# Optimization experiments

Hardware: AMD Instinct MI355X
Metric: run time of the kernel (lower is better)

Reference implementation:

```python
import jax, jax.numpy as jnp
import numpy as np

EPS = 0.25  # diffusion-map epsilon

def setup_inputs() -> dict:
    key = jax.random.key(0)
    ks = jax.random.split(key, 6)
    B, N, F, L = 8, 2048, 256, 16
    s = lambda fan_in: 1.0 / np.sqrt(fan_in)
    return {
        "x":      jax.random.normal(ks[0], (B, N, F), dtype=jnp.float32),
        "proj_w": jax.random.normal(ks[1], (L, F), dtype=jnp.float32) * s(F),
        "proj_b": jnp.zeros((L,), dtype=jnp.float32),
        "pi_w1":  jax.random.normal(ks[2], (F, L), dtype=jnp.float32) * s(L),
        "pi_b1":  jnp.zeros((F,), dtype=jnp.float32),
        "pi_w2":  jax.random.normal(ks[3], (1, F), dtype=jnp.float32) * s(F),
        "pi_b2":  jnp.zeros((1,), dtype=jnp.float32),
        "dt":     jnp.array([0.1], dtype=jnp.float32),
    }

def reference(x, proj_w, proj_b, pi_w1, pi_b1, pi_w2, pi_b2, dt):
    # z = proj(x): [B, N, L]
    z = jnp.einsum("bnf,lf->bnl", x, proj_w) + proj_b
    # pairwise squared distances via expansion (avoids [B,N,N,L] intermediate)
    sq = jnp.sum(z * z, axis=-1)                              # [B, N]
    gram = jnp.einsum("bnl,bml->bnm", z, z)                   # [B, N, N]
    d2 = jnp.maximum(sq[:, :, None] + sq[:, None, :] - 2.0 * gram, 0.0)
    K = jnp.exp(-d2 / (4.0 * EPS))                            # K_epsilon [B,N,N]
    q = jnp.sum(K, axis=2)                                    # q_epsilon_tilde [B,N]
    # pi(z): MLP 16 -> 256 -> 1 with ReLU then Sigmoid
    h = jax.nn.relu(jnp.einsum("bnl,fl->bnf", z, pi_w1) + pi_b1)
    pi_v = jax.nn.sigmoid(jnp.einsum("bnf,of->bno", h, pi_w2) + pi_b2)[..., 0]  # [B,N]
    # K_tilde = K @ diag(pi/q): scale columns
    Kt = K * (pi_v / q)[:, None, :]                            # [B,N,N]
    row = jnp.sum(Kt, axis=2) + 1e-5                           # diag of D_tilde
    # L = (1/eps) * D_tilde^{-1} K_tilde - I ; inverse of diagonal = reciprocal
    # L @ x computed without materializing identity:
    Lx = (1.0 / EPS) * jnp.einsum("bnm,bmf->bnf", Kt / row[:, :, None], x) - x
    return x + dt[0] * Lx
```

## Files before the change

### kernel.cpp

```cpp
#include <hip/hip_runtime.h>
#include <hip/hip_bf16.h>

#define BATCH 8
#define NN    2048
#define FF    256
#define LL    16

typedef float f32x4 __attribute__((ext_vector_type(4)));
typedef short s16x8 __attribute__((ext_vector_type(8)));

static __device__ __forceinline__ unsigned short f2bf(float f) {
    return __builtin_bit_cast(unsigned short, __float2bfloat16(f));
}
static __device__ __forceinline__ float bf2f(unsigned short u) {
    unsigned int x = ((unsigned int)u) << 16;
    return __builtin_bit_cast(float, x);
}

__global__ __launch_bounds__(256) void fused_a_kernel(
    const float* __restrict__ x,
    const float* __restrict__ proj_w, const float* __restrict__ proj_b,
    const float* __restrict__ pi_w1,  const float* __restrict__ pi_b1,
    const float* __restrict__ pi_w2,  const float* __restrict__ pi_b2,
    unsigned short* __restrict__ xT,
    unsigned short* __restrict__ zbG,
    float* __restrict__ sqbuf,
    float* __restrict__ pibuf)
{
    const int bid = blockIdx.x;
    const int b = bid & 7, nt = bid >> 3;
    const int n0 = nt * 32;
    const int t = threadIdx.x;
    const int wv = t >> 6, ln = t & 63;
    const int kg = ln >> 4, cl = ln & 15;

    const float* xb = x + (size_t)b * NN * FF;
    unsigned short* xTb = xT + (size_t)b * FF * NN;

    __shared__ unsigned short xbsh[32 * 264];
    __shared__ unsigned short Wbsh[16 * 264];
    __shared__ unsigned short W1bsh[256 * 24];
    __shared__ unsigned short zbsh[32 * 24];
    __shared__ float b1sh[256], w2sh[256], pbsh[16];
    __shared__ float pp[2][32];

#pragma unroll
    for (int i = 0; i < 8; ++i) {
        const int slot = i * 256 + t;
        const int r = slot >> 6, c4 = slot & 63;
        const float4 v = *(const float4*)(xb + (size_t)(n0 + r) * FF + c4 * 4);
        ushort4 o; o.x = f2bf(v.x); o.y = f2bf(v.y); o.z = f2bf(v.z); o.w = f2bf(v.w);
        *(ushort4*)&xbsh[r * 264 + c4 * 4] = o;
    }
#pragma unroll
    for (int i = 0; i < 4; ++i) {
        const int slot = i * 256 + t;
        const int l = slot >> 6, c4 = slot & 63;
        const float4 v = *(const float4*)(proj_w + l * FF + c4 * 4);
        ushort4 o; o.x = f2bf(v.x); o.y = f2bf(v.y); o.z = f2bf(v.z); o.w = f2bf(v.w);
        *(ushort4*)&Wbsh[l * 264 + c4 * 4] = o;
    }
#pragma unroll
    for (int i = 0; i < 4; ++i) {
        const int slot = i * 256 + t;
        const int f = slot >> 2, q = slot & 3;
        const float4 v = *(const float4*)(pi_w1 + f * LL + q * 4);
        ushort4 o; o.x = f2bf(v.x); o.y = f2bf(v.y); o.z = f2bf(v.z); o.w = f2bf(v.w);
        *(ushort4*)&W1bsh[f * 24 + q * 4] = o;
    }
    b1sh[t] = pi_b1[t];
    w2sh[t] = pi_w2[t];
    if (t < 16) pbsh[t] = proj_b[t];
    __syncthreads();

    if (wv < 2) {
        f32x4 zacc = {0.f, 0.f, 0.f, 0.f};
#pragma unroll
        for (int g = 0; g < 8; ++g) {
            const s16x8 af = *(const s16x8*)&xbsh[(wv * 16 + cl) * 264 + g * 32 + kg * 8];
            const s16x8 bf = *(const s16x8*)&Wbsh[cl * 264 + g * 32 + kg * 8];
            zacc = __builtin_amdgcn_mfma_f32_16x16x32_bf16(af, bf, zacc, 0, 0, 0);
        }
        const float pb = pbsh[cl];
#pragma unroll
        for (int r = 0; r < 4; ++r)
            zbsh[(wv * 16 + kg * 4 + r) * 24 + cl] = f2bf(zacc[r] + pb);
    }
    __syncthreads();

    if (t < 32) {
        unsigned short zr[16]; float sq = 0.f;
#pragma unroll
        for (int l = 0; l < 16; ++l) {
            zr[l] = zbsh[t * 24 + l];
            const float zf = bf2f(zr[l]);
            sq = fmaf(zf, zf, sq);
        }
        unsigned short* dst = zbG + ((size_t)b * NN + n0 + t) * 16;
        *(uint4*)dst = *(uint4*)&zr[0];
        *(uint4*)(dst + 8) = *(uint4*)&zr[8];
        sqbuf[(size_t)b * NN + n0 + t] = sq;
    }

    {
        const int ntl = wv & 1;
        s16x8 bz = {0, 0, 0, 0, 0, 0, 0, 0};
        if (kg < 2) bz = *(const s16x8*)&zbsh[(ntl * 16 + cl) * 24 + kg * 8];
        float pisum = 0.f;
        const f32x4 zf4 = {0.f, 0.f, 0.f, 0.f};
#pragma unroll
        for (int j = 0; j < 8; ++j) {
            const int ft = (wv >> 1) * 8 + j;
            s16x8 aw = {0, 0, 0, 0, 0, 0, 0, 0};
            if (kg < 2) aw = *(const s16x8*)&W1bsh[(ft * 16 + cl) * 24 + kg * 8];
            const f32x4 h4 = __builtin_amdgcn_mfma_f32_16x16x32_bf16(aw, bz, zf4, 0, 0, 0);
#pragma unroll
            for (int r = 0; r < 4; ++r) {
                const int f = ft * 16 + kg * 4 + r;
                const float h = fmaxf(h4[r] + b1sh[f], 0.f);
                pisum = fmaf(h, w2sh[f], pisum);
            }
        }
        pisum += __shfl_xor(pisum, 16, 64);
        pisum += __shfl_xor(pisum, 32, 64);
        if (ln < 16) pp[wv >> 1][ntl * 16 + ln] = pisum;
    }
    __syncthreads();

    if (t < 32) {
        const float tp = pp[0][t] + pp[1][t] + pi_b2[0];
        pibuf[(size_t)b * NN + n0 + t] = 1.f / (1.f + __expf(-tp));
    }

#pragma unroll
    for (int it = 0; it < 8; ++it) {
        const int f = wv * 64 + it * 8 + (ln >> 3);
        const int q = ln & 7;
        ushort4 o;
        o.x = xbsh[(q * 4 + 0) * 264 + f];
        o.y = xbsh[(q * 4 + 1) * 264 + f];
        o.z = xbsh[(q * 4 + 2) * 264 + f];
        o.w = xbsh[(q * 4 + 3) * 264 + f];
        *(ushort4*)(xTb + (size_t)f * NN + n0 + q * 4) = o;
    }
}

__global__ __launch_bounds__(256) void qc_kernel(
    const unsigned short* __restrict__ zbG,
    const float* __restrict__ sqbuf,
    const float* __restrict__ pibuf,
    float* __restrict__ cbuf)
{
    const int bid = blockIdx.x;
    const int b = bid & 7, nt = bid >> 3;
    const int n0 = nt * 32;
    const int t = threadIdx.x;
    const int wv = t >> 6, ln = t & 63;
    const int kg = ln >> 4, cl = ln & 15;

    const unsigned short* zb = zbG + (size_t)b * NN * LL;
    const float* sqb = sqbuf + (size_t)b * NN;
    __shared__ float qq[2][32];

    s16x8 zn = {0, 0, 0, 0, 0, 0, 0, 0};
    if (kg < 2) zn = *(const s16x8*)(zb + (size_t)(n0 + (wv & 1) * 16 + cl) * 16 + kg * 8);
    const float sqn = sqb[n0 + (wv & 1) * 16 + cl];
    const f32x4 zf4 = {0.f, 0.f, 0.f, 0.f};
    float qloc = 0.f;

#pragma unroll 2
    for (int ch = 0; ch < 32; ++ch) {
#pragma unroll
        for (int mi = 0; mi < 2; ++mi) {
            const int mm = ch * 64 + ((wv >> 1) + mi * 2) * 16;
            s16x8 zm = {0, 0, 0, 0, 0, 0, 0, 0};
            if (kg < 2) zm = *(const s16x8*)(zb + (size_t)(mm + cl) * 16 + kg * 8);
            const f32x4 sqm4 = *(const f32x4*)(sqb + mm + kg * 4);
            const f32x4 g = __builtin_amdgcn_mfma_f32_16x16x32_bf16(zm, zn, zf4, 0, 0, 0);
#pragma unroll
            for (int r = 0; r < 4; ++r)
                qloc += __expf(2.f * g[r] - sqm4[r] - sqn);
        }
    }
    qloc += __shfl_xor(qloc, 16, 64);
    qloc += __shfl_xor(qloc, 32, 64);
    if (ln < 16) qq[wv >> 1][(wv & 1) * 16 + ln] = qloc;
    __syncthreads();
    if (t < 32) {
        const size_t gi = (size_t)b * NN + n0 + t;
        cbuf[gi] = pibuf[gi] / (qq[0][t] + qq[1][t]);
    }
}

struct MRegs {
    s16x8 zm0, zm1;
    f32x4 sqm0, sqm1, cm0, cm1;
    s16x8 a0, a1, a2, a3;
};

__global__ __launch_bounds__(512) void main_kernel(
    const float* __restrict__ x,
    const unsigned short* __restrict__ xT,
    const unsigned short* __restrict__ zbG,
    const float* __restrict__ sqbuf,
    const float* __restrict__ cbuf,
    const float* __restrict__ dtp,
    float* __restrict__ out)
{
    const int bid = blockIdx.x;
    const int b = bid & 7, nt = bid >> 3;
    const int n0 = nt * 64;
    const int t = threadIdx.x;
    const int wv = t >> 6, ln = t & 63;
    const int kg = ln >> 4, cl = ln & 15;
    const int nt4 = wv >> 1;
    const int mgrp = wv & 1;

    const float*          xb  = x   + (size_t)b * NN * FF;
    const unsigned short* xTb = xT  + (size_t)b * FF * NN;
    const unsigned short* zb  = zbG + (size_t)b * NN * LL;
    const float*          sqB = sqbuf + (size_t)b * NN;
    const float*          cB  = cbuf  + (size_t)b * NN;
    float*                ob  = out + (size_t)b * NN * FF;

    __shared__ unsigned short wsh[2][64][64];
    __shared__ float rsp[2][64];

    const float dtv = dtp[0];
    const int nloc = nt4 * 16 + cl;

    s16x8 zn = {0, 0, 0, 0, 0, 0, 0, 0};
    if (kg < 2) zn = *(const s16x8*)(zb + (size_t)(n0 + nloc) * 16 + kg * 8);
    const float sqn = sqB[n0 + nloc];
    const f32x4 zf4 = {0.f, 0.f, 0.f, 0.f};

    f32x4 acc[2][4];
#pragma unroll
    for (int fi = 0; fi < 2; ++fi)
#pragma unroll
        for (int ni = 0; ni < 4; ++ni) acc[fi][ni] = (f32x4){0.f, 0.f, 0.f, 0.f};
    float rloc = 0.f;

    auto PRE = [&](MRegs& R, int kt) {
        const int m0 = kt * 64;
        const int mmA = m0 + (mgrp * 2 + 0) * 16;
        const int mmB = m0 + (mgrp * 2 + 1) * 16;
        R.zm0 = (s16x8){0, 0, 0, 0, 0, 0, 0, 0};
        R.zm1 = (s16x8){0, 0, 0, 0, 0, 0, 0, 0};
        if (kg < 2) {
            R.zm0 = *(const s16x8*)(zb + (size_t)(mmA + cl) * 16 + kg * 8);
            R.zm1 = *(const s16x8*)(zb + (size_t)(mmB + cl) * 16 + kg * 8);
        }
        R.sqm0 = *(const f32x4*)(sqB + mmA + kg * 4);
        R.sqm1 = *(const f32x4*)(sqB + mmB + kg * 4);
        R.cm0  = *(const f32x4*)(cB + mmA + kg * 4);
        R.cm1  = *(const f32x4*)(cB + mmB + kg * 4);
        const unsigned short* xr0 = xTb + (size_t)(wv * 32 + cl) * NN + m0;
        const unsigned short* xr1 = xTb + (size_t)(wv * 32 + 16 + cl) * NN + m0;
        R.a0 = *(const s16x8*)(xr0 + kg * 8);
        R.a1 = *(const s16x8*)(xr1 + kg * 8);
        R.a2 = *(const s16x8*)(xr0 + 32 + kg * 8);
        R.a3 = *(const s16x8*)(xr1 + 32 + kg * 8);
    };

    auto P1 = [&](const MRegs& R, int cur) {
        char* wb = (char*)wsh + cur * 8192;
#pragma unroll
        for (int j = 0; j < 2; ++j) {
            const s16x8 zm  = j ? R.zm1  : R.zm0;
            const f32x4 sqm = j ? R.sqm1 : R.sqm0;
            const f32x4 cm  = j ? R.cm1  : R.cm0;
            const int mt = mgrp * 2 + j;
            const f32x4 g = __builtin_amdgcn_mfma_f32_16x16x32_bf16(zm, zn, zf4, 0, 0, 0);
            const float w0 = __expf(2.f * g[0] - sqm[0] - sqn) * cm[0];
            const float w1 = __expf(2.f * g[1] - sqm[1] - sqn) * cm[1];
            const float w2 = __expf(2.f * g[2] - sqm[2] - sqn) * cm[2];
            const float w3 = __expf(2.f * g[3] - sqm[3] - sqn) * cm[3];
            rloc += (w0 + w1) + (w2 + w3);
            uint2 val;
            val.x = (unsigned)f2bf(w0) | ((unsigned)f2bf(w1) << 16);
            val.y = (unsigned)f2bf(w2) | ((unsigned)f2bf(w3) << 16);
            const int c16 = mt * 2 + (kg >> 1);
            const int phys = c16 ^ (nloc & 7);
            *(uint2*)(wb + nloc * 128 + phys * 16 + (kg & 1) * 8) = val;
        }
    };

    auto P2 = [&](const MRegs& R, int cur) {
        const char* wb = (const char*)wsh + cur * 8192;
#pragma unroll
        for (int ks = 0; ks < 2; ++ks) {
            s16x8 bw[4];
#pragma unroll
            for (int ni = 0; ni < 4; ++ni) {
                const int nr = ni * 16 + cl;
                const int phys = (ks * 4 + kg) ^ (nr & 7);
                bw[ni] = *(const s16x8*)(wb + nr * 128 + phys * 16);
            }
            const s16x8 aA = ks ? R.a2 : R.a0;
            const s16x8 aB = ks ? R.a3 : R.a1;
#pragma unroll
            for (int ni = 0; ni < 4; ++ni) {
                acc[0][ni] = __builtin_amdgcn_mfma_f32_16x16x32_bf16(aA, bw[ni], acc[0][ni], 0, 0, 0);
                acc[1][ni] = __builtin_amdgcn_mfma_f32_16x16x32_bf16(aB, bw[ni], acc[1][ni], 0, 0, 0);
            }
        }
    };

    MRegs rA, rB;
    PRE(rA, 0);
    for (int kt2 = 0; kt2 < 32; kt2 += 2) {
        PRE(rB, kt2 + 1);
        P1(rA, 0);
        __syncthreads();
        P2(rA, 0);
        if (kt2 + 2 < 32) PRE(rA, kt2 + 2);
        P1(rB, 1);
        __syncthreads();
        P2(rB, 1);
    }

    rloc += __shfl_xor(rloc, 16, 64);
    rloc += __shfl_xor(rloc, 32, 64);
    if (ln < 16) rsp[mgrp][nt4 * 16 + ln] = rloc;
    __syncthreads();

#pragma unroll
    for (int ni = 0; ni < 4; ++ni) {
        const int nl = ni * 16 + cl;
        const float rstot = rsp[0][nl] + rsp[1][nl] + 1e-5f;
        const float sc = 4.f * dtv / rstot;
        const int ng = n0 + nl;
#pragma unroll
        for (int fi = 0; fi < 2; ++fi) {
            const int fg = wv * 32 + fi * 16 + kg * 4;
            const float4 xv = *(const float4*)(xb + (size_t)ng * FF + fg);
            float4 o;
            o.x = (1.f - dtv) * xv.x + sc * acc[fi][ni][0];
            o.y = (1.f - dtv) * xv.y + sc * acc[fi][ni][1];
            o.z = (1.f - dtv) * xv.z + sc * acc[fi][ni][2];
            o.w = (1.f - dtv) * xv.w + sc * acc[fi][ni][3];
            *(float4*)(ob + (size_t)ng * FF + fg) = o;
        }
    }
}

extern "C" void kernel_launch(void* const* d_in, const int* in_sizes, int n_in,
                              void* d_out, int out_size, void* d_ws, size_t ws_size,
                              hipStream_t stream) {
    const float* x      = (const float*)d_in[0];
    const float* proj_w = (const float*)d_in[1];
    const float* proj_b = (const float*)d_in[2];
    const float* pi_w1  = (const float*)d_in[3];
    const float* pi_b1  = (const float*)d_in[4];
    const float* pi_w2  = (const float*)d_in[5];
    const float* pi_b2  = (const float*)d_in[6];
    const float* dtp    = (const float*)d_in[7];
    float* out = (float*)d_out;

    unsigned short* xT  = (unsigned short*)d_ws;
    unsigned short* zbG = xT + (size_t)BATCH * FF * NN;
    float* sqbuf = (float*)(zbG + (size_t)BATCH * NN * LL);
    float* pibuf = sqbuf + (size_t)BATCH * NN;
    float* cbuf  = pibuf + (size_t)BATCH * NN;

    fused_a_kernel<<<dim3(BATCH * (NN / 32)), dim3(256), 0, stream>>>(
        x, proj_w, proj_b, pi_w1, pi_b1, pi_w2, pi_b2, xT, zbG, sqbuf, pibuf);

    qc_kernel<<<dim3(BATCH * (NN / 32)), dim3(256), 0, stream>>>(
        zbG, sqbuf, pibuf, cbuf);

    main_kernel<<<dim3(BATCH * (NN / 64)), dim3(512), 0, stream>>>(
        x, xT, zbG, sqbuf, cbuf, dtp, out);
}
```

Measured before the change: 153.8 us.

## Split main kernel over feature halves, stage xT via async global-to-LDS loads

The main kernel now runs twice as many 256-thread blocks, each covering 128 of the 256 features. Each block stages xT tiles into swizzled LDS with global_load_lds and raises wave priority around the MFMA phase. The qc kernel double-buffers z and squared norms through LDS instead of reading them per tile from global memory. The fused_a kernel pads its LDS rows and moves the transpose write onto the otherwise idle waves. The cost is that every block recomputes the full kernel weights and row sums for its rows, doubling the exp work in the main kernel.

```diff
diff --git a/kernel.cpp b/kernel.cpp
--- a/kernel.cpp
+++ b/kernel.cpp
@@ -15,6 +15,12 @@
 static __device__ __forceinline__ float bf2f(unsigned short u) {
     unsigned int x = ((unsigned int)u) << 16;
     return __builtin_bit_cast(float, x);
+}
+
+typedef const __attribute__((address_space(1))) unsigned int glb_uint;
+typedef __attribute__((address_space(3))) unsigned int lds_uint;
+static __device__ __forceinline__ void gload_lds16(const void* g, void* l) {
+    __builtin_amdgcn_global_load_lds((glb_uint*)g, (lds_uint*)l, 16, 0, 0);
 }
 
 __global__ __launch_bounds__(256) void fused_a_kernel(
@@ -37,8 +43,8 @@
     const float* xb = x + (size_t)b * NN * FF;
     unsigned short* xTb = xT + (size_t)b * FF * NN;
 
-    __shared__ unsigned short xbsh[32 * 264];
-    __shared__ unsigned short Wbsh[16 * 264];
+    __shared__ unsigned short xbsh[32 * 268];
+    __shared__ unsigned short Wbsh[16 * 268];
     __shared__ unsigned short W1bsh[256 * 24];
     __shared__ unsigned short zbsh[32 * 24];
     __shared__ float b1sh[256], w2sh[256], pbsh[16];
@@ -50,7 +56,7 @@
         const int r = slot >> 6, c4 = slot & 63;
         const float4 v = *(const float4*)(xb + (size_t)(n0 + r) * FF + c4 * 4);
         ushort4 o; o.x = f2bf(v.x); o.y = f2bf(v.y); o.z = f2bf(v.z); o.w = f2bf(v.w);
-        *(ushort4*)&xbsh[r * 264 + c4 * 4] = o;
+        *(ushort4*)&xbsh[r * 268 + c4 * 4] = o;
     }
 #pragma unroll
     for (int i = 0; i < 4; ++i) {
@@ -58,7 +64,7 @@
         const int l = slot >> 6, c4 = slot & 63;
         const float4 v = *(const float4*)(proj_w + l * FF + c4 * 4);
         ushort4 o; o.x = f2bf(v.x); o.y = f2bf(v.y); o.z = f2bf(v.z); o.w = f2bf(v.w);
-        *(ushort4*)&Wbsh[l * 264 + c4 * 4] = o;
+        *(ushort4*)&Wbsh[l * 268 + c4 * 4] = o;
     }
 #pragma unroll
     for (int i = 0; i < 4; ++i) {
@@ -77,14 +83,26 @@
         f32x4 zacc = {0.f, 0.f, 0.f, 0.f};
 #pragma unroll
         for (int g = 0; g < 8; ++g) {
-            const s16x8 af = *(const s16x8*)&xbsh[(wv * 16 + cl) * 264 + g * 32 + kg * 8];
-            const s16x8 bf = *(const s16x8*)&Wbsh[cl * 264 + g * 32 + kg * 8];
+            const s16x8 af = *(const s16x8*)&xbsh[(wv * 16 + cl) * 268 + g * 32 + kg * 8];
+            const s16x8 bf = *(const s16x8*)&Wbsh[cl * 268 + g * 32 + kg * 8];
             zacc = __builtin_amdgcn_mfma_f32_16x16x32_bf16(af, bf, zacc, 0, 0, 0);
         }
         const float pb = pbsh[cl];
 #pragma unroll
         for (int r = 0; r < 4; ++r)
             zbsh[(wv * 16 + kg * 4 + r) * 24 + cl] = f2bf(zacc[r] + pb);
+    } else {
+#pragma unroll
+        for (int it = 0; it < 16; ++it) {
+            const int f = (wv - 2) * 128 + it * 8 + (ln >> 3);
+            const int q = ln & 7;
+            ushort4 o;
+            o.x = xbsh[(q * 4 + 0) * 268 + f];
+            o.y = xbsh[(q * 4 + 1) * 268 + f];
+            o.z = xbsh[(q * 4 + 2) * 268 + f];
+            o.w = xbsh[(q * 4 + 3) * 268 + f];
+            *(ushort4*)(xTb + (size_t)f * NN + n0 + q * 4) = o;
+        }
     }
     __syncthreads();
 
@@ -130,18 +148,6 @@
     if (t < 32) {
         const float tp = pp[0][t] + pp[1][t] + pi_b2[0];
         pibuf[(size_t)b * NN + n0 + t] = 1.f / (1.f + __expf(-tp));
-    }
-
-#pragma unroll
-    for (int it = 0; it < 8; ++it) {
-        const int f = wv * 64 + it * 8 + (ln >> 3);
-        const int q = ln & 7;
-        ushort4 o;
-        o.x = xbsh[(q * 4 + 0) * 264 + f];
-        o.y = xbsh[(q * 4 + 1) * 264 + f];
-        o.z = xbsh[(q * 4 + 2) * 264 + f];
-        o.w = xbsh[(q * 4 + 3) * 264 + f];
-        *(ushort4*)(xTb + (size_t)f * NN + n0 + q * 4) = o;
     }
 }
 
@@ -160,6 +166,9 @@
 
     const unsigned short* zb = zbG + (size_t)b * NN * LL;
     const float* sqb = sqbuf + (size_t)b * NN;
+
+    __shared__ unsigned short zsh[2][256 * 24];
+    __shared__ float sqh[2][256];
     __shared__ float qq[2][32];
 
     s16x8 zn = {0, 0, 0, 0, 0, 0, 0, 0};
@@ -168,19 +177,39 @@
     const f32x4 zf4 = {0.f, 0.f, 0.f, 0.f};
     float qloc = 0.f;
 
-#pragma unroll 2
-    for (int ch = 0; ch < 32; ++ch) {
-#pragma unroll
-        for (int mi = 0; mi < 2; ++mi) {
-            const int mm = ch * 64 + ((wv >> 1) + mi * 2) * 16;
+    uint4 za = *(const uint4*)(zb + (size_t)t * 16);
+    uint4 zc = *(const uint4*)(zb + (size_t)t * 16 + 8);
+    float sv = sqb[t];
+    *(uint4*)&zsh[0][t * 24] = za;
+    *(uint4*)&zsh[0][t * 24 + 8] = zc;
+    sqh[0][t] = sv;
+    __syncthreads();
+
+    const int mbase = (wv >> 1) * 128;
+    for (int ch = 0; ch < 8; ++ch) {
+        const int cur = ch & 1;
+        if (ch < 7) {
+            const int m = (ch + 1) * 256 + t;
+            za = *(const uint4*)(zb + (size_t)m * 16);
+            zc = *(const uint4*)(zb + (size_t)m * 16 + 8);
+            sv = sqb[m];
+        }
+#pragma unroll
+        for (int mt = 0; mt < 8; ++mt) {
             s16x8 zm = {0, 0, 0, 0, 0, 0, 0, 0};
-            if (kg < 2) zm = *(const s16x8*)(zb + (size_t)(mm + cl) * 16 + kg * 8);
-            const f32x4 sqm4 = *(const f32x4*)(sqb + mm + kg * 4);
+            if (kg < 2) zm = *(const s16x8*)&zsh[cur][(mbase + mt * 16 + cl) * 24 + kg * 8];
             const f32x4 g = __builtin_amdgcn_mfma_f32_16x16x32_bf16(zm, zn, zf4, 0, 0, 0);
+            const f32x4 sq4 = *(const f32x4*)&sqh[cur][mbase + mt * 16 + kg * 4];
 #pragma unroll
             for (int r = 0; r < 4; ++r)
-                qloc += __expf(2.f * g[r] - sqm4[r] - sqn);
-        }
+                qloc += __expf(2.f * g[r] - sq4[r] - sqn);
+        }
+        if (ch < 7) {
+            *(uint4*)&zsh[cur ^ 1][t * 24] = za;
+            *(uint4*)&zsh[cur ^ 1][t * 24 + 8] = zc;
+            sqh[cur ^ 1][t] = sv;
+        }
+        __syncthreads();
     }
     qloc += __shfl_xor(qloc, 16, 64);
     qloc += __shfl_xor(qloc, 32, 64);
@@ -192,13 +221,9 @@
     }
 }
 
-struct MRegs {
-    s16x8 zm0, zm1;
-    f32x4 sqm0, sqm1, cm0, cm1;
-    s16x8 a0, a1, a2, a3;
-};
-
-__global__ __launch_bounds__(512) void main_kernel(
+struct ZM { s16x8 z[4]; };
+
+__global__ __launch_bounds__(256) void main_kernel(
     const float* __restrict__ x,
     const unsigned short* __restrict__ xT,
     const unsigned short* __restrict__ zbG,
@@ -208,13 +233,14 @@
     float* __restrict__ out)
 {
     const int bid = blockIdx.x;
-    const int b = bid & 7, nt = bid >> 3;
-    const int n0 = nt * 64;
+    const int b = bid & 7;
+    const int rest = bid >> 3;
+    const int fs = rest & 1;
+    const int nt = rest >> 1;
+    const int n0 = nt * 64, f0 = fs * 128;
     const int t = threadIdx.x;
     const int wv = t >> 6, ln = t & 63;
     const int kg = ln >> 4, cl = ln & 15;
-    const int nt4 = wv >> 1;
-    const int mgrp = wv & 1;
 
     const float*          xb  = x   + (size_t)b * NN * FF;
     const unsigned short* xTb = xT  + (size_t)b * FF * NN;
@@ -223,11 +249,13 @@
     const float*          cB  = cbuf  + (size_t)b * NN;
     float*                ob  = out + (size_t)b * NN * FF;
 
-    __shared__ unsigned short wsh[2][64][64];
-    __shared__ float rsp[2][64];
+    __shared__ unsigned short xsh[2][128 * 64];
+    __shared__ unsigned short wsh[2][64 * 64];
+    __shared__ float csh[2][64], sqsh[2][64];
+    __shared__ float rsp[64];
 
     const float dtv = dtp[0];
-    const int nloc = nt4 * 16 + cl;
+    const int nloc = wv * 16 + cl;
 
     s16x8 zn = {0, 0, 0, 0, 0, 0, 0, 0};
     if (kg < 2) zn = *(const s16x8*)(zb + (size_t)(n0 + nloc) * 16 + kg * 8);
@@ -241,41 +269,43 @@
         for (int ni = 0; ni < 4; ++ni) acc[fi][ni] = (f32x4){0.f, 0.f, 0.f, 0.f};
     float rloc = 0.f;
 
-    auto PRE = [&](MRegs& R, int kt) {
+    auto loadZM = [&](ZM& Z, int kt) {
         const int m0 = kt * 64;
-        const int mmA = m0 + (mgrp * 2 + 0) * 16;
-        const int mmB = m0 + (mgrp * 2 + 1) * 16;
-        R.zm0 = (s16x8){0, 0, 0, 0, 0, 0, 0, 0};
-        R.zm1 = (s16x8){0, 0, 0, 0, 0, 0, 0, 0};
-        if (kg < 2) {
-            R.zm0 = *(const s16x8*)(zb + (size_t)(mmA + cl) * 16 + kg * 8);
-            R.zm1 = *(const s16x8*)(zb + (size_t)(mmB + cl) * 16 + kg * 8);
-        }
-        R.sqm0 = *(const f32x4*)(sqB + mmA + kg * 4);
-        R.sqm1 = *(const f32x4*)(sqB + mmB + kg * 4);
-        R.cm0  = *(const f32x4*)(cB + mmA + kg * 4);
-        R.cm1  = *(const f32x4*)(cB + mmB + kg * 4);
-        const unsigned short* xr0 = xTb + (size_t)(wv * 32 + cl) * NN + m0;
-        const unsigned short* xr1 = xTb + (size_t)(wv * 32 + 16 + cl) * NN + m0;
-        R.a0 = *(const s16x8*)(xr0 + kg * 8);
-        R.a1 = *(const s16x8*)(xr1 + kg * 8);
-        R.a2 = *(const s16x8*)(xr0 + 32 + kg * 8);
-        R.a3 = *(const s16x8*)(xr1 + 32 + kg * 8);
+#pragma unroll
+        for (int mt = 0; mt < 4; ++mt) {
+            Z.z[mt] = (s16x8){0, 0, 0, 0, 0, 0, 0, 0};
+            if (kg < 2)
+                Z.z[mt] = *(const s16x8*)(zb + (size_t)(m0 + mt * 16 + cl) * 16 + kg * 8);
+        }
     };
-
-    auto P1 = [&](const MRegs& R, int cur) {
-        char* wb = (char*)wsh + cur * 8192;
-#pragma unroll
-        for (int j = 0; j < 2; ++j) {
-            const s16x8 zm  = j ? R.zm1  : R.zm0;
-            const f32x4 sqm = j ? R.sqm1 : R.sqm0;
-            const f32x4 cm  = j ? R.cm1  : R.cm0;
-            const int mt = mgrp * 2 + j;
-            const f32x4 g = __builtin_amdgcn_mfma_f32_16x16x32_bf16(zm, zn, zf4, 0, 0, 0);
-            const float w0 = __expf(2.f * g[0] - sqm[0] - sqn) * cm[0];
-            const float w1 = __expf(2.f * g[1] - sqm[1] - sqn) * cm[1];
-            const float w2 = __expf(2.f * g[2] - sqm[2] - sqn) * cm[2];
-            const float w3 = __expf(2.f * g[3] - sqm[3] - sqn) * cm[3];
+    auto STAGE_CS = [&](int buf, int kt) {
+        const int m0 = kt * 64;
+        if (t < 64)        csh[buf][t]       = cB[m0 + t];
+        else if (t < 128)  sqsh[buf][t - 64] = sqB[m0 + t - 64];
+    };
+    auto ISSUE = [&](int buf, int kt) {
+        const int m0 = kt * 64;
+        char* dst = (char*)&xsh[buf][0];
+#pragma unroll
+        for (int i = 0; i < 4; ++i) {
+            const int fl = (i * 4 + wv) * 8 + (ln >> 3);
+            const int cp = ln & 7;
+            const int clog = cp ^ (fl & 7);
+            const unsigned short* src = xTb + (size_t)(f0 + fl) * NN + m0 + clog * 8;
+            gload_lds16(src, dst + (i * 4 + wv) * 1024);
+        }
+    };
+    auto P1 = [&](const ZM& Z, int cur) {
+        char* wb = (char*)&wsh[cur][0];
+#pragma unroll
+        for (int mt = 0; mt < 4; ++mt) {
+            const f32x4 g = __builtin_amdgcn_mfma_f32_16x16x32_bf16(Z.z[mt], zn, zf4, 0, 0, 0);
+            const f32x4 sq4 = *(const f32x4*)&sqsh[cur][mt * 16 + kg * 4];
+            const f32x4 cm4 = *(const f32x4*)&csh[cur][mt * 16 + kg * 4];
+            const float w0 = __expf(2.f * g[0] - sq4[0] - sqn) * cm4[0];
+            const float w1 = __expf(2.f * g[1] - sq4[1] - sqn) * cm4[1];
+            const float w2 = __expf(2.f * g[2] - sq4[2] - sqn) * cm4[2];
+            const float w3 = __expf(2.f * g[3] - sq4[3] - sqn) * cm4[3];
             rloc += (w0 + w1) + (w2 + w3);
             uint2 val;
             val.x = (unsigned)f2bf(w0) | ((unsigned)f2bf(w1) << 16);
@@ -285,55 +315,69 @@
             *(uint2*)(wb + nloc * 128 + phys * 16 + (kg & 1) * 8) = val;
         }
     };
-
-    auto P2 = [&](const MRegs& R, int cur) {
-        const char* wb = (const char*)wsh + cur * 8192;
+    auto P2 = [&](int cur) {
+        const char* xbuf = (const char*)&xsh[cur][0];
+        const char* wbuf = (const char*)&wsh[cur][0];
 #pragma unroll
         for (int ks = 0; ks < 2; ++ks) {
-            s16x8 bw[4];
+            s16x8 a[2], bw[4];
+#pragma unroll
+            for (int fi = 0; fi < 2; ++fi) {
+                const int fl = wv * 32 + fi * 16 + cl;
+                const int slot = (ks * 4 + kg) ^ (fl & 7);
+                a[fi] = *(const s16x8*)(xbuf + fl * 128 + slot * 16);
+            }
 #pragma unroll
             for (int ni = 0; ni < 4; ++ni) {
                 const int nr = ni * 16 + cl;
-                const int phys = (ks * 4 + kg) ^ (nr & 7);
-                bw[ni] = *(const s16x8*)(wb + nr * 128 + phys * 16);
+                const int slot = (ks * 4 + kg) ^ (nr & 7);
+                bw[ni] = *(const s16x8*)(wbuf + nr * 128 + slot * 16);
             }
-            const s16x8 aA = ks ? R.a2 : R.a0;
-            const s16x8 aB = ks ? R.a3 : R.a1;
-#pragma unroll
-            for (int ni = 0; ni < 4; ++ni) {
-                acc[0][ni] = __builtin_amdgcn_mfma_f32_16x16x32_bf16(aA, bw[ni], acc[0][ni], 0, 0, 0);
-                acc[1][ni] = __builtin_amdgcn_mfma_f32_16x16x32_bf16(aB, bw[ni], acc[1][ni], 0, 0, 0);
-            }
+#pragma unroll
+            for (int fi = 0; fi < 2; ++fi)
+#pragma unroll
+                for (int ni = 0; ni < 4; ++ni)
+                    acc[fi][ni] = __builtin_amdgcn_mfma_f32_16x16x32_bf16(
+                        a[fi], bw[ni], acc[fi][ni], 0, 0, 0);
         }
     };
 
-    MRegs rA, rB;
-    PRE(rA, 0);
-    for (int kt2 = 0; kt2 < 32; kt2 += 2) {
-        PRE(rB, kt2 + 1);
-        P1(rA, 0);
+    ZM zA, zB;
+    STAGE_CS(0, 0);
+    loadZM(zA, 0);
+    ISSUE(0, 0);
+    __syncthreads();
+
+    for (int kt = 0; kt < 32; kt += 2) {
+        P1(zA, 0);
+        { loadZM(zB, kt + 1); STAGE_CS(1, kt + 1); }
         __syncthreads();
-        P2(rA, 0);
-        if (kt2 + 2 < 32) PRE(rA, kt2 + 2);
-        P1(rB, 1);
+        ISSUE(1, kt + 1);
+        __builtin_amdgcn_s_setprio(1);
+        P2(0);
+        __builtin_amdgcn_s_setprio(0);
+        P1(zB, 1);
+        if (kt + 2 < 32) { loadZM(zA, kt + 2); STAGE_CS(0, kt + 2); }
         __syncthreads();
-        P2(rB, 1);
+        if (kt + 2 < 32) ISSUE(0, kt + 2);
+        __builtin_amdgcn_s_setprio(1);
+        P2(1);
+        __builtin_amdgcn_s_setprio(0);
     }
 
     rloc += __shfl_xor(rloc, 16, 64);
     rloc += __shfl_xor(rloc, 32, 64);
-    if (ln < 16) rsp[mgrp][nt4 * 16 + ln] = rloc;
+    if (ln < 16) rsp[wv * 16 + ln] = rloc;
     __syncthreads();
 
 #pragma unroll
     for (int ni = 0; ni < 4; ++ni) {
         const int nl = ni * 16 + cl;
-        const float rstot = rsp[0][nl] + rsp[1][nl] + 1e-5f;
-        const float sc = 4.f * dtv / rstot;
+        const float sc = 4.f * dtv / (rsp[nl] + 1e-5f);
         const int ng = n0 + nl;
 #pragma unroll
         for (int fi = 0; fi < 2; ++fi) {
-            const int fg = wv * 32 + fi * 16 + kg * 4;
+            const int fg = f0 + wv * 32 + fi * 16 + kg * 4;
             const float4 xv = *(const float4*)(xb + (size_t)ng * FF + fg);
             float4 o;
             o.x = (1.f - dtv) * xv.x + sc * acc[fi][ni][0];
@@ -370,6 +414,6 @@
     qc_kernel<<<dim3(BATCH * (NN / 32)), dim3(256), 0, stream>>>(
         zbG, sqbuf, pibuf, cbuf);
 
-    main_kernel<<<dim3(BATCH * (NN / 64)), dim3(512), 0, stream>>>(
+    main_kernel<<<dim3(BATCH * (NN / 64) * 2), dim3(256), 0, stream>>>(
         x, xT, zbG, sqbuf, cbuf, dtp, out);
 }
```

Result: faster. 148.3 us (-3.5%).
